# Optimization experiments

Hardware: AMD Instinct MI355X
Metric: run time of the kernel (lower is better)

Reference implementation:

```python
import jax, jax.numpy as jnp
import numpy as np

CUTOFFS = [0, 20000, 40000, 50000]
B, S, D = 2, 1024, 256

def setup_inputs() -> dict:
    key = jax.random.key(0)
    ks = jax.random.split(key, 6)
    x = jax.random.normal(ks[0], (B, S, D), dtype=jnp.float32)
    targets = jax.random.randint(ks[1], (B, S), 0, CUTOFFS[-1], dtype=jnp.int64)
    scale = 1.0 / np.sqrt(D)
    w0 = jax.random.normal(ks[2], (CUTOFFS[1] - CUTOFFS[0], D), dtype=jnp.float32) * scale
    w1 = jax.random.normal(ks[3], (CUTOFFS[2] - CUTOFFS[1], D), dtype=jnp.float32) * scale
    w2 = jax.random.normal(ks[4], (CUTOFFS[3] - CUTOFFS[2], D), dtype=jnp.float32) * scale
    b0 = jnp.zeros((CUTOFFS[1] - CUTOFFS[0],), dtype=jnp.float32)
    b1 = jnp.zeros((CUTOFFS[2] - CUTOFFS[1],), dtype=jnp.float32)
    b2 = jnp.zeros((CUTOFFS[3] - CUTOFFS[2],), dtype=jnp.float32)
    return {"x": x, "targets": targets, "w0": w0, "w1": w1, "w2": w2,
            "b0": b0, "b1": b1, "b2": b2}

def reference(x, targets, w0, w1, w2, b0, b1, b2):
    # Faithful to TF: for each cluster, compute dense logits for ALL tokens,
    # zero out positions whose target id is outside [l, r) (scatter_nd of the
    # boolean-masked logits into a zeros tensor == multiply by mask), concat
    # along vocab, then log_softmax over the full vocab.
    ws = [w0, w1, w2]
    bs = [b0, b1, b2]
    pieces = []
    for i in range(len(CUTOFFS) - 1):
        l, r = CUTOFFS[i], CUTOFFS[i + 1]
        mask = ((targets >= l) & (targets < r)).astype(x.dtype)[..., None]  # [B,S,1]
        logits = jnp.einsum('bsd,vd->bsv', x, ws[i]) + bs[i]               # [B,S,r-l]
        pieces.append(logits * mask)
    out = jnp.concatenate(pieces, axis=-1)  # [B,S,n_token]
    return jax.nn.log_softmax(out, axis=-1)
```

## Files before the change

### kernel.cpp

```cpp
#include <hip/hip_runtime.h>
#include <hip/hip_bf16.h>
#include <math.h>


typedef __attribute__((ext_vector_type(4))) float f32x4;
typedef __attribute__((ext_vector_type(8))) short bf16x8;
typedef __attribute__((ext_vector_type(4))) unsigned short u16x4;

#define PSTRIDE 320

__device__ __forceinline__ unsigned int f2bf(float f) {
    union { float f; unsigned int u; } cv; cv.f = f;
    unsigned int u = cv.u + 0x7fffu + ((cv.u >> 16) & 1u);
    return u >> 16;
}
__device__ __forceinline__ float bf2f(unsigned short h) {
    union { unsigned int u; float f; } cv; cv.u = ((unsigned int)h) << 16;
    return cv.f;
}

__global__ __launch_bounds__(1024) void classify_kernel(
    const int* __restrict__ targets, int* cnt, int* lists,
    int n_tok, int c1, int c2) {
    __shared__ int lcnt[3];
    int tid = threadIdx.x;
    if (tid < 3) lcnt[tid] = 0;
    __syncthreads();
    for (int t = tid; t < n_tok; t += 1024) {
        int tgt = targets[t];
        int c = (tgt < c1) ? 0 : ((tgt < c2) ? 1 : 2);
        int pos = atomicAdd(&lcnt[c], 1);
        lists[c * n_tok + pos] = t;
    }
    __syncthreads();
    if (tid < 3) cnt[tid] = lcnt[tid];
}

__global__ __launch_bounds__(512) void pack_a_kernel(
    const float* __restrict__ x, const int* __restrict__ lists,
    const int* __restrict__ cnt, unsigned short* __restrict__ packA,
    int n_tok) {
    int it0 = (cnt[0] + 255) >> 8, it1 = (cnt[1] + 255) >> 8,
        it2 = (cnt[2] + 255) >> 8;
    int g0 = it0 * 16, g1 = it1 * 16, g2 = it2 * 16;
    int gb = blockIdx.x;
    int c, g, n, base;
    if (gb < g0)                { c = 0; g = gb;            n = cnt[0]; base = 0; }
    else if (gb < g0 + g1)      { c = 1; g = gb - g0;       n = cnt[1]; base = g0; }
    else if (gb < g0 + g1 + g2) { c = 2; g = gb - g0 - g1;  n = cnt[2]; base = g0 + g1; }
    else return;

    int tid = threadIdx.x;
    int k0 = tid >> 6, lane = tid & 63;
    int l15 = lane & 15, lg = lane >> 4;
    int pos = g * 16 + l15;
    int tok = (pos < n) ? lists[c * n_tok + pos] : -1;
    uint4 pk = make_uint4(0u, 0u, 0u, 0u);
    if (tok >= 0) {
        const float* src = x + (size_t)tok * 256 + k0 * 32 + lg * 8;
        float4 lo = *(const float4*)src;
        float4 hi = *(const float4*)(src + 4);
        pk.x = f2bf(lo.x) | (f2bf(lo.y) << 16);
        pk.y = f2bf(lo.z) | (f2bf(lo.w) << 16);
        pk.z = f2bf(hi.x) | (f2bf(hi.y) << 16);
        pk.w = f2bf(hi.z) | (f2bf(hi.w) << 16);
    }
    *(uint4*)(packA + ((size_t)(base + g) * 8 + k0) * 512 + lane * 8) = pk;
}

__global__ __launch_bounds__(256, 4) void gemm_ws_kernel(
    const unsigned short* __restrict__ packA,
    const float* __restrict__ w0, const float* __restrict__ w1,
    const float* __restrict__ w2,
    const float* __restrict__ b0, const float* __restrict__ b1,
    const float* __restrict__ b2,
    const int* __restrict__ lists, const int* __restrict__ cnt,
    int V0, int V1, int V2, int nv0, int nv1,
    unsigned short* __restrict__ lws, int lstride,
    float* __restrict__ psum, int n_tok, int N) {

    __shared__ __align__(16) unsigned char wlds[64 * 512];
    __shared__ int tok_lds[2048];

    int bid = blockIdx.x;
    int c, vt;
    if (bid < nv0)            { c = 0; vt = bid; }
    else if (bid < nv0 + nv1) { c = 1; vt = bid - nv0; }
    else                      { c = 2; vt = bid - nv0 - nv1; }

    const float* Wc; const float* Bc; int Vc;
    if (c == 0)      { Wc = w0; Bc = b0; Vc = V0; }
    else if (c == 1) { Wc = w1; Bc = b1; Vc = V1; }
    else             { Wc = w2; Bc = b2; Vc = V2; }

    int it0 = (cnt[0] + 255) >> 8, it1 = (cnt[1] + 255) >> 8;
    int baseg = (c == 0) ? 0 : ((c == 1) ? it0 * 16 : (it0 + it1) * 16);

    int n = cnt[c];
    int nIter = (n + 255) >> 8;
    int v0 = vt * 64;
    int tid = threadIdx.x;

    #pragma unroll
    for (int u0 = 0; u0 < 2; ++u0) {
        int u = u0 * 256 + tid;
        int row = u >> 3, seg = u & 7;
        int v = v0 + row;
        float4 f[8];
        if (v < Vc) {
            const float* src = Wc + (size_t)v * 256 + seg * 32;
            #pragma unroll
            for (int j = 0; j < 8; ++j) f[j] = *(const float4*)(src + j * 4);
        } else {
            #pragma unroll
            for (int j = 0; j < 8; ++j) f[j] = make_float4(0.f, 0.f, 0.f, 0.f);
        }
        unsigned fb = (unsigned)(((row >> 4) * 8 + seg) * 1024);
        int l15r = row & 15;
        #pragma unroll
        for (int j = 0; j < 4; ++j) {
            uint4 pk;
            pk.x = f2bf(f[2*j].x)   | (f2bf(f[2*j].y)   << 16);
            pk.y = f2bf(f[2*j].z)   | (f2bf(f[2*j].w)   << 16);
            pk.z = f2bf(f[2*j+1].x) | (f2bf(f[2*j+1].y) << 16);
            pk.w = f2bf(f[2*j+1].z) | (f2bf(f[2*j+1].w) << 16);
            *(uint4*)(wlds + fb + (j * 16 + l15r) * 16) = pk;
        }
    }
    for (int i = tid; i < nIter * 256; i += 256)
        tok_lds[i] = (i < n) ? lists[c * n_tok + i] : -1;
    __syncthreads();

    int lane = tid & 63;
    int wid  = tid >> 6;
    int lg = lane >> 4, l15 = lane & 15;
    const char* pA = (const char*)packA;

    float bv[4];
    #pragma unroll
    for (int nn = 0; nn < 4; ++nn) {
        int vl = v0 + nn * 16 + l15;
        bv[nn] = (vl < Vc) ? Bc[vl] : -__builtin_huge_valf();
    }

    for (int it = 0; it < nIter; ++it) {
        int tb = it * 256 + wid * 64;
        if (tb >= n) continue;
        const char* ga = pA + (size_t)(baseg + it * 16 + wid * 4) * 8192 + lane * 16;

        f32x4 acc[4][4];
        #pragma unroll
        for (int m = 0; m < 4; ++m)
            #pragma unroll
            for (int nn = 0; nn < 4; ++nn)
                acc[m][nn] = (f32x4){0.f, 0.f, 0.f, 0.f};

        #pragma unroll
        for (int k0 = 0; k0 < 8; ++k0) {
            bf16x8 a[4], b[4];
            #pragma unroll
            for (int m = 0; m < 4; ++m)
                a[m] = *(const bf16x8*)(ga + m * 8192 + k0 * 1024);
            #pragma unroll
            for (int nn = 0; nn < 4; ++nn)
                b[nn] = *(const bf16x8*)(wlds + (nn * 8 + k0) * 1024 + lane * 16);
            #pragma unroll
            for (int m = 0; m < 4; ++m)
                #pragma unroll
                for (int nn = 0; nn < 4; ++nn)
                    acc[m][nn] = __builtin_amdgcn_mfma_f32_16x16x32_bf16(
                        a[m], b[nn], acc[m][nn], 0, 0, 0);
        }

        #pragma unroll
        for (int m = 0; m < 4; ++m) {
            #pragma unroll
            for (int rr = 0; rr < 4; ++rr) {
                int tokid = tok_lds[tb + m * 16 + lg * 4 + rr];
                float s = 0.f;
                unsigned short* dst =
                    lws + (size_t)(tokid < 0 ? 0 : tokid) * lstride + v0 + l15;
                #pragma unroll
                for (int nn = 0; nn < 4; ++nn) {
                    float lgt = acc[m][nn][rr] + bv[nn];
                    s += __expf(lgt);
                    if (tokid >= 0)
                        dst[nn * 16] = (unsigned short)f2bf(lgt);
                }
                s += __shfl_xor(s, 1); s += __shfl_xor(s, 2);
                s += __shfl_xor(s, 4); s += __shfl_xor(s, 8);
                if (tokid >= 0 && l15 == 0)
                    psum[(size_t)tokid * PSTRIDE + vt] = s;
            }
        }
    }
}

__global__ __launch_bounds__(256) void finalize_kernel(
    float* __restrict__ out, const unsigned short* __restrict__ lws,
    int lstride, const int* __restrict__ targets,
    const float* __restrict__ psum, int c1, int c2, int N) {
    int t = blockIdx.x;
    int tid = threadIdx.x;
    int tgt = targets[t];
    int l, r, V;
    if (tgt < c1)      { l = 0;  r = c1; V = c1; }
    else if (tgt < c2) { l = c1; r = c2; V = c2 - c1; }
    else               { l = c2; r = N;  V = N - c2; }

    int nv = (V + 63) >> 6;
    const float* p = psum + (size_t)t * PSTRIDE;
    float s = 0.f;
    for (int i = tid; i < nv; i += 256) s += p[i];
    s += __shfl_down(s, 32); s += __shfl_down(s, 16); s += __shfl_down(s, 8);
    s += __shfl_down(s, 4);  s += __shfl_down(s, 2);  s += __shfl_down(s, 1);
    __shared__ float sred[4];
    __shared__ float sL;
    if ((tid & 63) == 0) sred[tid >> 6] = s;
    __syncthreads();
    if (tid == 0)
        sL = logf(sred[0] + sred[1] + sred[2] + sred[3] + (float)(N - V));
    __syncthreads();
    float L = sL;

    float* orow = out + (size_t)t * N;
    const unsigned short* lrow = lws + (size_t)t * lstride;
    f32x4 neg = (f32x4){-L, -L, -L, -L};
    for (int i4 = tid * 4; i4 < N; i4 += 1024) {
        f32x4 res;
        if (i4 >= l && i4 < r) {
            u16x4 u = *(const u16x4*)(lrow + (i4 - l));
            res = (f32x4){bf2f(u.x) - L, bf2f(u.y) - L,
                          bf2f(u.z) - L, bf2f(u.w) - L};
        } else {
            res = neg;
        }
        __builtin_nontemporal_store(res, (f32x4*)(orow + i4));
    }
}

extern "C" void kernel_launch(void* const* d_in, const int* in_sizes, int n_in,
                              void* d_out, int out_size, void* d_ws, size_t ws_size,
                              hipStream_t stream) {
    const float* x       = (const float*)d_in[0];
    const int*   targets = (const int*)d_in[1];
    const float* w0      = (const float*)d_in[2];
    const float* w1      = (const float*)d_in[3];
    const float* w2      = (const float*)d_in[4];
    const float* b0      = (const float*)d_in[5];
    const float* b1      = (const float*)d_in[6];
    const float* b2      = (const float*)d_in[7];
    float* out = (float*)d_out;

    int n_tok = in_sizes[1];
    int V0 = in_sizes[5];
    int V1 = in_sizes[6];
    int V2 = in_sizes[7];
    int N  = V0 + V1 + V2;
    int c1 = V0, c2 = V0 + V1;
    int nv0 = (V0 + 63) >> 6, nv1 = (V1 + 63) >> 6, nv2 = (V2 + 63) >> 6;
    int maxV = V0 > V1 ? V0 : V1; if (V2 > maxV) maxV = V2;
    int lstride = ((maxV + 63) >> 6) << 6;

    int maxGroups = (((n_tok + 255) >> 8) << 4) + 32;

    char* ws = (char*)d_ws;
    size_t off = 0;
    int* cnt = (int*)(ws + off);      off += 256;
    int* lists = (int*)(ws + off);    off += (((size_t)3 * n_tok * 4 + 255) & ~(size_t)255);
    float* psum = (float*)(ws + off); off += (((size_t)n_tok * PSTRIDE * 4 + 255) & ~(size_t)255);
    unsigned short* packA = (unsigned short*)(ws + off);
    off += (((size_t)maxGroups * 8192 + 255) & ~(size_t)255);
    unsigned short* lws = (unsigned short*)(ws + off);

    classify_kernel<<<1, 1024, 0, stream>>>(targets, cnt, lists, n_tok, c1, c2);

    pack_a_kernel<<<maxGroups, 512, 0, stream>>>(x, lists, cnt, packA, n_tok);

    gemm_ws_kernel<<<nv0 + nv1 + nv2, 256, 0, stream>>>(
        packA, w0, w1, w2, b0, b1, b2, lists, cnt,
        V0, V1, V2, nv0, nv1, lws, lstride, psum, n_tok, N);

    finalize_kernel<<<n_tok, 256, 0, stream>>>(
        out, lws, lstride, targets, psum, c1, c2, N);
}
```

Before: 156.8 us.

## Move softmax exp-sum from GEMM epilogue into finalize using LDS-staged rows

```diff
diff --git a/kernel.cpp b/kernel.cpp
--- a/kernel.cpp
+++ b/kernel.cpp
@@ -6,8 +6,7 @@
 typedef __attribute__((ext_vector_type(4))) float f32x4;
 typedef __attribute__((ext_vector_type(8))) short bf16x8;
 typedef __attribute__((ext_vector_type(4))) unsigned short u16x4;
-
-#define PSTRIDE 320
+typedef __attribute__((ext_vector_type(8))) unsigned short u16x8;
 
 __device__ __forceinline__ unsigned int f2bf(float f) {
     union { float f; unsigned int u; } cv; cv.f = f;
@@ -76,8 +75,7 @@
     const float* __restrict__ b2,
     const int* __restrict__ lists, const int* __restrict__ cnt,
     int V0, int V1, int V2, int nv0, int nv1,
-    unsigned short* __restrict__ lws, int lstride,
-    float* __restrict__ psum, int n_tok, int N) {
+    unsigned short* __restrict__ lws, int lstride, int n_tok) {
 
     __shared__ __align__(16) unsigned char wlds[64 * 512];
     __shared__ int tok_lds[2048];
@@ -177,20 +175,14 @@
             #pragma unroll
             for (int rr = 0; rr < 4; ++rr) {
                 int tokid = tok_lds[tb + m * 16 + lg * 4 + rr];
-                float s = 0.f;
-                unsigned short* dst =
-                    lws + (size_t)(tokid < 0 ? 0 : tokid) * lstride + v0 + l15;
-                #pragma unroll
-                for (int nn = 0; nn < 4; ++nn) {
-                    float lgt = acc[m][nn][rr] + bv[nn];
-                    s += __expf(lgt);
-                    if (tokid >= 0)
-                        dst[nn * 16] = (unsigned short)f2bf(lgt);
+                if (tokid >= 0) {
+                    unsigned short* dst =
+                        lws + (size_t)tokid * lstride + v0 + l15;
+                    #pragma unroll
+                    for (int nn = 0; nn < 4; ++nn)
+                        dst[nn * 16] =
+                            (unsigned short)f2bf(acc[m][nn][rr] + bv[nn]);
                 }
-                s += __shfl_xor(s, 1); s += __shfl_xor(s, 2);
-                s += __shfl_xor(s, 4); s += __shfl_xor(s, 8);
-                if (tokid >= 0 && l15 == 0)
-                    psum[(size_t)tokid * PSTRIDE + vt] = s;
             }
         }
     }
@@ -198,8 +190,11 @@
 
 __global__ __launch_bounds__(256) void finalize_kernel(
     float* __restrict__ out, const unsigned short* __restrict__ lws,
-    int lstride, const int* __restrict__ targets,
-    const float* __restrict__ psum, int c1, int c2, int N) {
+    int lstride, const int* __restrict__ targets, int c1, int c2, int N) {
+    __shared__ unsigned short srow[20000];
+    __shared__ float sred[4];
+    __shared__ float sL;
+
     int t = blockIdx.x;
     int tid = threadIdx.x;
     int tgt = targets[t];
@@ -208,14 +203,21 @@
     else if (tgt < c2) { l = c1; r = c2; V = c2 - c1; }
     else               { l = c2; r = N;  V = N - c2; }
 
-    int nv = (V + 63) >> 6;
-    const float* p = psum + (size_t)t * PSTRIDE;
+    const unsigned short* lrow = lws + (size_t)t * lstride;
+    int Vp8 = (V + 7) & ~7;
+    bool lds_ok = (Vp8 <= 20000);
+
     float s = 0.f;
-    for (int i = tid; i < nv; i += 256) s += p[i];
+    for (int i = tid * 8; i < Vp8; i += 2048) {
+        u16x8 u = *(const u16x8*)(lrow + i);
+        if (lds_ok) *(u16x8*)(srow + i) = u;
+        s += __expf(bf2f(u.s0)) + __expf(bf2f(u.s1))
+           + __expf(bf2f(u.s2)) + __expf(bf2f(u.s3))
+           + __expf(bf2f(u.s4)) + __expf(bf2f(u.s5))
+           + __expf(bf2f(u.s6)) + __expf(bf2f(u.s7));
+    }
     s += __shfl_down(s, 32); s += __shfl_down(s, 16); s += __shfl_down(s, 8);
     s += __shfl_down(s, 4);  s += __shfl_down(s, 2);  s += __shfl_down(s, 1);
-    __shared__ float sred[4];
-    __shared__ float sL;
     if ((tid & 63) == 0) sred[tid >> 6] = s;
     __syncthreads();
     if (tid == 0)
@@ -224,12 +226,12 @@
     float L = sL;
 
     float* orow = out + (size_t)t * N;
-    const unsigned short* lrow = lws + (size_t)t * lstride;
     f32x4 neg = (f32x4){-L, -L, -L, -L};
     for (int i4 = tid * 4; i4 < N; i4 += 1024) {
         f32x4 res;
         if (i4 >= l && i4 < r) {
-            u16x4 u = *(const u16x4*)(lrow + (i4 - l));
+            u16x4 u = lds_ok ? *(const u16x4*)(srow + (i4 - l))
+                             : *(const u16x4*)(lrow + (i4 - l));
             res = (f32x4){bf2f(u.x) - L, bf2f(u.y) - L,
                           bf2f(u.z) - L, bf2f(u.w) - L};
         } else {
@@ -262,13 +264,12 @@
     int maxV = V0 > V1 ? V0 : V1; if (V2 > maxV) maxV = V2;
     int lstride = ((maxV + 63) >> 6) << 6;
 
-    int maxGroups = (((n_tok + 255) >> 8) << 4) + 32;
+    int maxGroups = (((n_tok + 255) >> 8) + 3) << 4;
 
     char* ws = (char*)d_ws;
     size_t off = 0;
     int* cnt = (int*)(ws + off);      off += 256;
     int* lists = (int*)(ws + off);    off += (((size_t)3 * n_tok * 4 + 255) & ~(size_t)255);
-    float* psum = (float*)(ws + off); off += (((size_t)n_tok * PSTRIDE * 4 + 255) & ~(size_t)255);
     unsigned short* packA = (unsigned short*)(ws + off);
     off += (((size_t)maxGroups * 8192 + 255) & ~(size_t)255);
     unsigned short* lws = (unsigned short*)(ws + off);
@@ -279,8 +280,8 @@
 
     gemm_ws_kernel<<<nv0 + nv1 + nv2, 256, 0, stream>>>(
         packA, w0, w1, w2, b0, b1, b2, lists, cnt,
-        V0, V1, V2, nv0, nv1, lws, lstride, psum, n_tok, N);
+        V0, V1, V2, nv0, nv1, lws, lstride, n_tok);
 
     finalize_kernel<<<n_tok, 256, 0, stream>>>(
-        out, lws, lstride, targets, psum, c1, c2, N);
-}
+        out, lws, lstride, targets, c1, c2, N);
+}
```

New measurement: 147.8 us. 1.06x faster.
